# Kernel optimization log

Hardware: AMD Instinct MI355X
Metric: run time of the kernel (lower is better)

Reference implementation:

```python
import jax, jax.numpy as jnp
import numpy as np

B, L, K = 4, 1024, 48
EF, NF, NPE, NRBF, NCLS = 128, 128, 16, 16, 3
MAXREL = 32
EDGE_IN = NPE + NRBF * 25  # 416


def setup_inputs():
    key = jax.random.key(0)
    ks = jax.random.split(key, 8)
    X = jax.random.normal(ks[0], (B, L, 4, 3), jnp.float32)
    mask = jnp.ones((B, L), jnp.float32)
    R_idx = jnp.arange(B * L, dtype=jnp.int64).reshape(B, L)
    chain_labels = jax.random.randint(ks[1], (B, L), 0, 4).astype(jnp.int64)
    membrane_per_residue_labels = jax.random.randint(ks[2], (B, L), 0, NCLS).astype(jnp.int64)
    pe_w = jax.random.normal(ks[3], (2 * MAXREL + 2, NPE), jnp.float32) * 0.05
    pe_b = jax.random.normal(ks[4], (NPE,), jnp.float32) * 0.05
    edge_w = jax.random.normal(ks[5], (EDGE_IN, EF), jnp.float32) * 0.05
    ne_g = jnp.ones((EF,), jnp.float32)
    ne_b = jnp.zeros((EF,), jnp.float32)
    node_w = jax.random.normal(ks[6], (NCLS, NF), jnp.float32) * 0.05
    nn_g = jnp.ones((NF,), jnp.float32)
    nn_b = jnp.zeros((NF,), jnp.float32)
    return {"X": X, "mask": mask, "R_idx": R_idx, "chain_labels": chain_labels,
            "membrane_per_residue_labels": membrane_per_residue_labels,
            "pe_w": pe_w, "pe_b": pe_b, "edge_w": edge_w, "ne_g": ne_g, "ne_b": ne_b,
            "node_w": node_w, "nn_g": nn_g, "nn_b": nn_b}


def _rbf(D):
    mu = jnp.linspace(2.0, 22.0, NRBF)
    sigma = (22.0 - 2.0) / NRBF
    return jnp.exp(-(((D[..., None] - mu) / sigma) ** 2))


def _gather_nb(v, e_idx):
    # v: [B, L, ...] -> [B, L, K, ...] gathered along residue dim
    return jax.vmap(lambda vi, ii: vi[ii])(v, e_idx)


def _ln(x, g, b, eps=1e-5):
    mu = jnp.mean(x, -1, keepdims=True)
    var = jnp.mean((x - mu) ** 2, -1, keepdims=True)
    return (x - mu) / jnp.sqrt(var + eps) * g + b


# 24 atom-pair RBFs after the Ca-Ca (D_neighbors) one, in the original concat order
PAIRS = [("N","N"),("C","C"),("O","O"),("Cb","Cb"),("Ca","N"),("Ca","C"),("Ca","O"),
         ("Ca","Cb"),("N","C"),("N","O"),("N","Cb"),("Cb","C"),("Cb","O"),("O","C"),
         ("N","Ca"),("C","Ca"),("O","Ca"),("Cb","Ca"),("C","N"),("O","N"),("Cb","N"),
         ("C","Cb"),("O","Cb"),("C","O")]


def reference(X, mask, R_idx, chain_labels, membrane_per_residue_labels,
              pe_w, pe_b, edge_w, ne_g, ne_b, node_w, nn_g, nn_b):
    Na, Ca, Cc, Oo = X[:, :, 0], X[:, :, 1], X[:, :, 2], X[:, :, 3]
    bvec = Ca - Na
    cvec = Cc - Ca
    avec = jnp.cross(bvec, cvec)
    Cb = -0.58273431 * avec + 0.56802827 * bvec - 0.54067466 * cvec + Ca
    coords = {"N": Na, "Ca": Ca, "C": Cc, "O": Oo, "Cb": Cb}

    # masked Ca-Ca distances + kNN (single NxN pass)
    mask2 = mask[:, :, None] * mask[:, None, :]
    dX = Ca[:, :, None, :] - Ca[:, None, :, :]
    D = mask2 * jnp.sqrt(jnp.sum(dX ** 2, -1) + 1e-6)
    D_max = jnp.max(D, -1, keepdims=True)
    D_adj = D + (1.0 - mask2) * D_max
    negD, E_idx = jax.lax.top_k(-D_adj, K)
    D_neighbors = -negD  # [B, L, K]

    # gather neighbor coords once, compute the 25 RBF features on N*K pairs only
    nb = {n: _gather_nb(v, E_idx) for n, v in coords.items()}  # [B, L, K, 3]
    rbf_list = [_rbf(D_neighbors)]
    for an, bn in PAIRS:
        d = jnp.sqrt(jnp.sum((coords[an][:, :, None, :] - nb[bn]) ** 2, -1) + 1e-6)
        rbf_list.append(_rbf(d))
    RBF_all = jnp.concatenate(rbf_list, -1)  # [B, L, K, 400]

    # positional encodings on gathered offsets / chain equality
    off = R_idx[:, :, None] - _gather_nb(R_idx, E_idx)           # [B, L, K]
    E_chains = (chain_labels[:, :, None] == _gather_nb(chain_labels, E_idx)).astype(jnp.int32)
    d = jnp.clip(off + MAXREL, 0, 2 * MAXREL).astype(jnp.int32) * E_chains + (1 - E_chains) * (2 * MAXREL + 1)
    d1h = jax.nn.one_hot(d, 2 * MAXREL + 2, dtype=jnp.float32)
    E_pos = d1h @ pe_w + pe_b                                     # [B, L, K, 16]

    E = jnp.concatenate([E_pos, RBF_all], -1) @ edge_w            # [B, L, K, 128]
    E = _ln(E, ne_g, ne_b)

    C1h = jax.nn.one_hot(membrane_per_residue_labels, NCLS, dtype=jnp.float32)
    V = _ln(C1h @ node_w, nn_g, nn_b)                             # [B, L, 128]
    return V, E, E_idx
```

## Files before the change

### kernel.cpp

```cpp
#include <hip/hip_runtime.h>
#include <math.h>

#define B_ 4
#define L_ 1024
#define K_ 48
#define EF_ 128
#define NF_ 128
#define NPE_ 16
#define NRBF_ 16
#define MAXREL_ 32
#define EDGE_IN_ 416

#define V_SIZE   (B_*L_*NF_)
#define E_OFF    (V_SIZE)
#define E_SIZE   (B_*L_*K_*EF_)
#define EIDX_OFF (E_OFF + E_SIZE)

#define XH_STRIDE 232
#define SE_STRIDE 132

typedef __attribute__((ext_vector_type(8))) short bf16x8;
typedef __attribute__((ext_vector_type(4))) float f32x4;
typedef __attribute__((ext_vector_type(4))) unsigned u32x4;

__device__ const int PA_[25] = {1, 0,2,3,4, 1,1,1,1, 0,0,0, 4,4, 3, 0,2,3,4, 2,3,4, 2,3, 2};
__device__ const int PB_[25] = {1, 0,2,3,4, 0,2,3,4, 2,3,4, 2,3, 2, 1,1,1,1, 0,0,0, 4,4, 3};

__device__ __forceinline__ unsigned short f2bf(float f){
    unsigned u = __float_as_uint(f);
    unsigned r = u + 0x7fffu + ((u >> 16) & 1u);
    return (unsigned short)(r >> 16);
}

__global__ __launch_bounds__(256) void wprep_kernel(const float* __restrict__ w,
                                                    unsigned short* __restrict__ wt)
{
    int idx = blockIdx.x * 256 + threadIdx.x;
    if (idx >= EDGE_IN_ * EF_) return;
    int f = idx & 127;
    int k = idx >> 7;
    wt[f * EDGE_IN_ + k] = f2bf(w[k * EF_ + f]);
}

__global__ __launch_bounds__(128) void v_kernel(const int* __restrict__ labels,
                                                const float* __restrict__ node_w,
                                                const float* __restrict__ g,
                                                const float* __restrict__ bb,
                                                float* __restrict__ out)
{
    int gi = blockIdx.x;
    int f  = threadIdx.x;
    int lbl = labels[gi];
    float v = node_w[lbl*NF_ + f];

    __shared__ float red[2];
    __shared__ float red2[2];
    float s = v;
    #pragma unroll
    for (int m = 1; m < 64; m <<= 1) s += __shfl_xor(s, m, 64);
    if ((f & 63) == 0) red[f >> 6] = s;
    __syncthreads();
    float mu = (red[0] + red[1]) * (1.0f / NF_);
    float d = v - mu;
    float s2 = d * d;
    #pragma unroll
    for (int m = 1; m < 64; m <<= 1) s2 += __shfl_xor(s2, m, 64);
    if ((f & 63) == 0) red2[f >> 6] = s2;
    __syncthreads();
    float var = (red2[0] + red2[1]) * (1.0f / NF_);
    out[gi*NF_ + f] = d * rsqrtf(var + 1e-5f) * g[f] + bb[f];
}

__global__ __launch_bounds__(256) void topk_kernel(const float* __restrict__ X,
                                                   const float* __restrict__ mask,
                                                   float* __restrict__ out)
{
    __shared__ float sCa[L_ * 3];
    __shared__ float sM[L_];
    __shared__ unsigned hist[256];
    __shared__ float wmax[4];
    __shared__ int sSelBin;
    __shared__ unsigned sSelLo;
    __shared__ unsigned long long cand[K_];
    __shared__ unsigned sCnt;

    int gi = blockIdx.x;
    int b  = gi >> 10;
    int i  = gi & (L_ - 1);
    int tid = threadIdx.x;

    for (int idx = tid; idx < L_ * 3; idx += 256) {
        int j = idx / 3, d = idx - j * 3;
        sCa[idx] = X[(((size_t)((b << 10) + j)) * 4 + 1) * 3 + d];
    }
    for (int j = tid; j < L_; j += 256) sM[j] = mask[(b << 10) + j];
    if (tid == 0) sCnt = 0;
    __syncthreads();

    float cx = sCa[i*3+0], cy = sCa[i*3+1], cz = sCa[i*3+2];
    float mi = sM[i];

    float lmax = 0.0f;
    #pragma unroll
    for (int q = 0; q < 4; ++q) {
        int j = tid + q * 256;
        float dx = cx - sCa[j*3+0];
        float dy = cy - sCa[j*3+1];
        float dz = cz - sCa[j*3+2];
        float dist = sqrtf(dx*dx + dy*dy + dz*dz + 1e-6f);
        lmax = fmaxf(lmax, mi * sM[j] * dist);
    }
    #pragma unroll
    for (int m = 1; m < 64; m <<= 1) lmax = fmaxf(lmax, __shfl_xor(lmax, m, 64));
    if ((tid & 63) == 0) wmax[tid >> 6] = lmax;
    __syncthreads();
    float Dmax = fmaxf(fmaxf(wmax[0], wmax[1]), fmaxf(wmax[2], wmax[3]));

    unsigned long long key[4];
    bool act[4];
    #pragma unroll
    for (int q = 0; q < 4; ++q) {
        int j = tid + q * 256;
        float dx = cx - sCa[j*3+0];
        float dy = cy - sCa[j*3+1];
        float dz = cz - sCa[j*3+2];
        float dist = sqrtf(dx*dx + dy*dy + dz*dz + 1e-6f);
        float m2 = mi * sM[j];
        float Dadj = m2 * dist + (1.0f - m2) * Dmax;
        key[q] = (((unsigned long long)__float_as_uint(Dadj)) << 32) | (unsigned)j;
        act[q] = true;
    }

    unsigned r = K_ - 1;
    unsigned long long T = 0;
    const int shifts[6] = {56, 48, 40, 32, 8, 0};
    #pragma unroll 1
    for (int p = 0; p < 6; ++p) {
        int sh = shifts[p];
        hist[tid] = 0;
        __syncthreads();
        #pragma unroll
        for (int q = 0; q < 4; ++q)
            if (act[q]) atomicAdd(&hist[(unsigned)((key[q] >> sh) & 255ULL)], 1u);
        __syncthreads();
        if (tid < 64) {
            unsigned b0 = hist[tid*4+0], b1 = hist[tid*4+1], b2 = hist[tid*4+2], b3 = hist[tid*4+3];
            unsigned s0 = b0, s1 = s0 + b1, s2 = s1 + b2, s3 = s2 + b3;
            unsigned s = s3;
            #pragma unroll
            for (int m = 1; m < 64; m <<= 1) {
                unsigned o = __shfl_up(s, m, 64);
                if (tid >= m) s += o;
            }
            unsigned base = s - s3;
            hist[tid*4+0] = base + s0;
            hist[tid*4+1] = base + s1;
            hist[tid*4+2] = base + s2;
            hist[tid*4+3] = base + s3;
        }
        __syncthreads();
        unsigned lo = (tid == 0) ? 0u : hist[tid - 1];
        unsigned hi = hist[tid];
        if (r >= lo && r < hi) { sSelBin = tid; sSelLo = lo; }
        __syncthreads();
        int bsel = sSelBin;
        r -= sSelLo;
        T |= ((unsigned long long)(unsigned)bsel) << sh;
        #pragma unroll
        for (int q = 0; q < 4; ++q)
            act[q] = act[q] && ((unsigned)((key[q] >> sh) & 255ULL) == (unsigned)bsel);
        __syncthreads();
    }

    #pragma unroll
    for (int q = 0; q < 4; ++q)
        if (key[q] <= T) {
            unsigned pos = atomicAdd(&sCnt, 1u);
            cand[pos] = key[q];
        }
    __syncthreads();

    if (tid < 64) {
        unsigned long long k64 = (tid < K_) ? cand[tid] : 0xffffffffffffffffULL;
        #pragma unroll
        for (unsigned kk = 2; kk <= 64; kk <<= 1) {
            #pragma unroll
            for (unsigned jj = kk >> 1; jj > 0; jj >>= 1) {
                unsigned long long o = __shfl_xor(k64, jj, 64);
                bool lower = (tid & jj) == 0;
                bool asc   = (tid & kk) == 0;
                unsigned long long mn = (k64 < o) ? k64 : o;
                unsigned long long mx = (k64 < o) ? o : k64;
                k64 = (lower == asc) ? mn : mx;
            }
        }
        if (tid < K_)
            out[EIDX_OFF + (size_t)gi * K_ + tid] = (float)(unsigned)(k64 & 0xffffffffULL);
    }
}

__global__ __launch_bounds__(256, 5) void edge_kernel(const float* __restrict__ X,
                                                   const int* __restrict__ Ridx,
                                                   const int* __restrict__ chains,
                                                   const float* __restrict__ pe_w,
                                                   const float* __restrict__ pe_b,
                                                   const unsigned short* __restrict__ wt,
                                                   const float* __restrict__ ne_g,
                                                   const float* __restrict__ ne_b,
                                                   float* __restrict__ out)
{
    __shared__ float sAI[16];
    __shared__ float sAJ[K_][16];
    __shared__ int   sJ[K_];
    __shared__ int   sDpos[K_];
    __shared__ __align__(16) unsigned char sBuf[K_ * SE_STRIDE * 4];

    unsigned short* xh = (unsigned short*)sBuf;
    float* sE = (float*)sBuf;

    int tid = threadIdx.x;
    int gi  = blockIdx.x;
    int b   = gi >> 10;
    int i   = gi & (L_ - 1);

    if (tid < K_) sJ[tid] = (int)out[EIDX_OFF + (size_t)gi * K_ + tid];
    __syncthreads();

    if (tid < K_ + 1) {
        int r = (tid < K_) ? sJ[tid] : i;
        const float* xr = X + ((size_t)((b << 10) + r)) * 12;
        float n0=xr[0],  n1=xr[1],  n2=xr[2];
        float a0=xr[3],  a1=xr[4],  a2=xr[5];
        float c0=xr[6],  c1=xr[7],  c2=xr[8];
        float o0=xr[9],  o1=xr[10], o2=xr[11];
        float bx=a0-n0, by=a1-n1, bz=a2-n2;
        float vx=c0-a0, vy=c1-a1, vz=c2-a2;
        float ax = by*vz - bz*vy;
        float ay = bz*vx - bx*vz;
        float az = bx*vy - by*vx;
        float cb0 = -0.58273431f*ax + 0.56802827f*bx - 0.54067466f*vx + a0;
        float cb1 = -0.58273431f*ay + 0.56802827f*by - 0.54067466f*vy + a1;
        float cb2 = -0.58273431f*az + 0.56802827f*bz - 0.54067466f*vz + a2;
        float* dst = (tid < K_) ? &sAJ[tid][0] : &sAI[0];
        dst[0]=n0;  dst[1]=n1;  dst[2]=n2;
        dst[3]=a0;  dst[4]=a1;  dst[5]=a2;
        dst[6]=c0;  dst[7]=c1;  dst[8]=c2;
        dst[9]=o0;  dst[10]=o1; dst[11]=o2;
        dst[12]=cb0; dst[13]=cb1; dst[14]=cb2;
    }
    if (tid >= 64 && tid < 64 + K_) {
        int e = tid - 64;
        int j = sJ[e];
        int off  = Ridx[gi] - Ridx[(b << 10) + j];
        int same = (chains[gi] == chains[(b << 10) + j]);
        int dcl = off + MAXREL_;
        dcl = dcl < 0 ? 0 : (dcl > 2*MAXREL_ ? 2*MAXREL_ : dcl);
        sDpos[e] = same ? dcl : (2*MAXREL_ + 1);
    }
    __syncthreads();

    const int wv = tid >> 6;
    const int ln = tid & 63;
    const int lr = ln & 15;
    const int lg = ln >> 4;

    f32x4 acc[3][2];
    #pragma unroll
    for (int rf = 0; rf < 3; ++rf)
        #pragma unroll
        for (int cf = 0; cf < 2; ++cf)
            acc[rf][cf] = (f32x4){0.0f, 0.0f, 0.0f, 0.0f};

    const unsigned short* wbase0 = wt + (size_t)(wv*32 + lr) * EDGE_IN_ + lg*8;
    const unsigned short* wbase1 = wt + (size_t)(wv*32 + 16 + lr) * EDGE_IN_ + lg*8;

    #pragma unroll
    for (int h = 0; h < 2; ++h) {
        if (h == 0) {
            #pragma unroll
            for (int p = 0; p < 2; ++p) {
                int idx = tid + p * 256;
                if (idx < 384) {
                    int e = idx >> 3, cc = (idx & 7) * 2;
                    int dp = sDpos[e];
                    float v0 = pe_w[dp*NPE_ + cc]     + pe_b[cc];
                    float v1 = pe_w[dp*NPE_ + cc + 1] + pe_b[cc + 1];
                    unsigned pk;
                    asm("v_cvt_pk_bf16_f32 %0, %1, %2" : "=v"(pk) : "v"(v0), "v"(v1));
                    *(unsigned*)&xh[e * XH_STRIDE + cc] = pk;
                }
            }
            #pragma unroll
            for (int p = 0; p < 3; ++p) {
                int idx = tid + p * 256;
                if (idx < 624) {
                    int e = idx / 13, g2 = idx - e * 13;
                    float dx = sAI[PA_[g2]*3+0] - sAJ[e][PB_[g2]*3+0];
                    float dy = sAI[PA_[g2]*3+1] - sAJ[e][PB_[g2]*3+1];
                    float dz = sAI[PA_[g2]*3+2] - sAJ[e][PB_[g2]*3+2];
                    float dist = sqrtf(dx*dx + dy*dy + dz*dz + 1e-6f);
                    float t = 0.8f * dist - 1.6f;
                    unsigned pk[8];
                    #pragma unroll
                    for (int rr = 0; rr < 8; ++rr) {
                        float v0 = __expf(-t * t); t -= 1.06666672f;
                        float v1 = __expf(-t * t); t -= 1.06666672f;
                        asm("v_cvt_pk_bf16_f32 %0, %1, %2" : "=v"(pk[rr]) : "v"(v0), "v"(v1));
                    }
                    u32x4 w0 = {pk[0], pk[1], pk[2], pk[3]};
                    u32x4 w1 = {pk[4], pk[5], pk[6], pk[7]};
                    int cb = NPE_ + g2 * 16;
                    *(u32x4*)&xh[e * XH_STRIDE + cb]     = w0;
                    *(u32x4*)&xh[e * XH_STRIDE + cb + 8] = w1;
                }
            }
        } else {
            #pragma unroll
            for (int p = 0; p < 3; ++p) {
                int idx = tid + p * 256;
                if (idx < 576) {
                    int e = idx / 12, g2 = 13 + (idx - e * 12);
                    float dx = sAI[PA_[g2]*3+0] - sAJ[e][PB_[g2]*3+0];
                    float dy = sAI[PA_[g2]*3+1] - sAJ[e][PB_[g2]*3+1];
                    float dz = sAI[PA_[g2]*3+2] - sAJ[e][PB_[g2]*3+2];
                    float dist = sqrtf(dx*dx + dy*dy + dz*dz + 1e-6f);
                    float t = 0.8f * dist - 1.6f;
                    unsigned pk[8];
                    #pragma unroll
                    for (int rr = 0; rr < 8; ++rr) {
                        float v0 = __expf(-t * t); t -= 1.06666672f;
                        float v1 = __expf(-t * t); t -= 1.06666672f;
                        asm("v_cvt_pk_bf16_f32 %0, %1, %2" : "=v"(pk[rr]) : "v"(v0), "v"(v1));
                    }
                    u32x4 w0 = {pk[0], pk[1], pk[2], pk[3]};
                    u32x4 w1 = {pk[4], pk[5], pk[6], pk[7]};
                    int cb = (g2 - 13) * 16;
                    *(u32x4*)&xh[e * XH_STRIDE + cb]     = w0;
                    *(u32x4*)&xh[e * XH_STRIDE + cb + 8] = w1;
                }
            }
        }
        __syncthreads();

        const int kb  = h ? 224 : 0;
        const int nks = h ? 6 : 7;
        #pragma unroll 4
        for (int ks = 0; ks < nks; ++ks) {
            int k0 = ks * 32;
            bf16x8 a[3], bh[2];
            bh[0] = *(const bf16x8*)(wbase0 + kb + k0);
            bh[1] = *(const bf16x8*)(wbase1 + kb + k0);
            #pragma unroll
            for (int rf = 0; rf < 3; ++rf)
                a[rf] = *(const bf16x8*)&xh[(rf*16 + lr) * XH_STRIDE + k0 + lg*8];
            #pragma unroll
            for (int rf = 0; rf < 3; ++rf) {
                #pragma unroll
                for (int cf = 0; cf < 2; ++cf)
                    acc[rf][cf] = __builtin_amdgcn_mfma_f32_16x16x32_bf16(a[rf], bh[cf], acc[rf][cf], 0, 0, 0);
            }
        }
        __syncthreads();
    }

    #pragma unroll
    for (int rf = 0; rf < 3; ++rf)
        #pragma unroll
        for (int cf = 0; cf < 2; ++cf)
            #pragma unroll
            for (int r = 0; r < 4; ++r) {
                int row = rf*16 + lg*4 + r;
                int col = wv*32 + cf*16 + lr;
                sE[row * SE_STRIDE + col] = acc[rf][cf][r];
            }
    __syncthreads();

    int l16 = tid & 15;
    float gv[8], bv[8];
    #pragma unroll
    for (int q = 0; q < 8; ++q) { gv[q] = ne_g[l16*8 + q]; bv[q] = ne_b[l16*8 + q]; }

    for (int p = 0; p < 3; ++p) {
        int e = p*16 + (tid >> 4);
        float vals[8];
        #pragma unroll
        for (int q = 0; q < 8; ++q) vals[q] = sE[e * SE_STRIDE + l16*8 + q];
        float sum = 0.0f;
        #pragma unroll
        for (int q = 0; q < 8; ++q) sum += vals[q];
        #pragma unroll
        for (int m = 1; m < 16; m <<= 1) sum += __shfl_xor(sum, m, 64);
        float mu = sum * (1.0f / 128.0f);
        float s2 = 0.0f;
        #pragma unroll
        for (int q = 0; q < 8; ++q) { float d = vals[q] - mu; s2 += d * d; }
        #pragma unroll
        for (int m = 1; m < 16; m <<= 1) s2 += __shfl_xor(s2, m, 64);
        float rstd = rsqrtf(s2 * (1.0f / 128.0f) + 1e-5f);

        float* dst = out + E_OFF + (size_t)(gi * K_ + e) * EF_ + l16*8;
        f32x4 o0, o1;
        o0[0] = (vals[0] - mu) * rstd * gv[0] + bv[0];
        o0[1] = (vals[1] - mu) * rstd * gv[1] + bv[1];
        o0[2] = (vals[2] - mu) * rstd * gv[2] + bv[2];
        o0[3] = (vals[3] - mu) * rstd * gv[3] + bv[3];
        o1[0] = (vals[4] - mu) * rstd * gv[4] + bv[4];
        o1[1] = (vals[5] - mu) * rstd * gv[5] + bv[5];
        o1[2] = (vals[6] - mu) * rstd * gv[6] + bv[6];
        o1[3] = (vals[7] - mu) * rstd * gv[7] + bv[7];
        __builtin_nontemporal_store(o0, (f32x4*)dst);
        __builtin_nontemporal_store(o1, (f32x4*)(dst + 4));
    }
}

extern "C" void kernel_launch(void* const* d_in, const int* in_sizes, int n_in,
                              void* d_out, int out_size, void* d_ws, size_t ws_size,
                              hipStream_t stream)
{
    const float* X      = (const float*)d_in[0];
    const float* mask   = (const float*)d_in[1];
    const int*   Ridx   = (const int*)d_in[2];
    const int*   chains = (const int*)d_in[3];
    const int*   memb   = (const int*)d_in[4];
    const float* pe_w   = (const float*)d_in[5];
    const float* pe_b   = (const float*)d_in[6];
    const float* edge_w = (const float*)d_in[7];
    const float* ne_g   = (const float*)d_in[8];
    const float* ne_b   = (const float*)d_in[9];
    const float* node_w = (const float*)d_in[10];
    const float* nn_g   = (const float*)d_in[11];
    const float* nn_b   = (const float*)d_in[12];
    float* out = (float*)d_out;

    unsigned short* wt = (unsigned short*)d_ws;

    wprep_kernel<<<(EDGE_IN_*EF_ + 255)/256, 256, 0, stream>>>(edge_w, wt);
    v_kernel<<<B_*L_, 128, 0, stream>>>(memb, node_w, nn_g, nn_b, out);
    topk_kernel<<<B_*L_, 256, 0, stream>>>(X, mask, out);
    edge_kernel<<<B_*L_, 256, 0, stream>>>(X, Ridx, chains, pe_w, pe_b,
                                           wt, ne_g, ne_b, out);
}
```

Measured before the change: 101.9 us.

## Fuse top-k and edge kernels into one per-residue kernel with early radix exit

Merges the top-k neighbour selection kernel and the edge featurization kernel into a single kernel per residue. The selected neighbour indices go to shared memory instead of being written to global memory and read back. The shared buffer is reused for the Ca coordinates, the mask and the edge staging, which keeps LDS use within the 5-blocks-per-CU launch bound. The radix select also stops early once the selected bin holds a single key. The cost is that the top-k phase now runs under the edge kernel's occupancy and register limits.

```diff
diff --git a/kernel.cpp b/kernel.cpp
--- a/kernel.cpp
+++ b/kernel.cpp
@@ -71,23 +71,39 @@
     out[gi*NF_ + f] = d * rsqrtf(var + 1e-5f) * g[f] + bb[f];
 }
 
-__global__ __launch_bounds__(256) void topk_kernel(const float* __restrict__ X,
+__global__ __launch_bounds__(256, 5) void fused_kernel(const float* __restrict__ X,
                                                    const float* __restrict__ mask,
+                                                   const int* __restrict__ Ridx,
+                                                   const int* __restrict__ chains,
+                                                   const float* __restrict__ pe_w,
+                                                   const float* __restrict__ pe_b,
+                                                   const unsigned short* __restrict__ wt,
+                                                   const float* __restrict__ ne_g,
+                                                   const float* __restrict__ ne_b,
                                                    float* __restrict__ out)
 {
-    __shared__ float sCa[L_ * 3];
-    __shared__ float sM[L_];
+    __shared__ __align__(16) unsigned char sBuf[K_ * SE_STRIDE * 4];
+    float* sCa = (float*)sBuf;
+    float* sM  = (float*)(sBuf + 12288);
+    unsigned short* xh = (unsigned short*)sBuf;
+    float* sE = (float*)sBuf;
+
+    __shared__ float sAI[16];
+    __shared__ float sAJ[K_][16];
+    __shared__ int   sJ[K_];
+    __shared__ int   sDpos[K_];
     __shared__ unsigned hist[256];
     __shared__ float wmax[4];
     __shared__ int sSelBin;
-    __shared__ unsigned sSelLo;
+    __shared__ unsigned sSelLo, sSelCnt;
+    __shared__ unsigned long long sTkey;
     __shared__ unsigned long long cand[K_];
     __shared__ unsigned sCnt;
 
-    int gi = blockIdx.x;
-    int b  = gi >> 10;
-    int i  = gi & (L_ - 1);
     int tid = threadIdx.x;
+    int gi  = blockIdx.x;
+    int b   = gi >> 10;
+    int i   = gi & (L_ - 1);
 
     for (int idx = tid; idx < L_ * 3; idx += 256) {
         int j = idx / 3, d = idx - j * 3;
@@ -161,7 +177,7 @@
         __syncthreads();
         unsigned lo = (tid == 0) ? 0u : hist[tid - 1];
         unsigned hi = hist[tid];
-        if (r >= lo && r < hi) { sSelBin = tid; sSelLo = lo; }
+        if (r >= lo && r < hi) { sSelBin = tid; sSelLo = lo; sSelCnt = hi - lo; }
         __syncthreads();
         int bsel = sSelBin;
         r -= sSelLo;
@@ -169,6 +185,14 @@
         #pragma unroll
         for (int q = 0; q < 4; ++q)
             act[q] = act[q] && ((unsigned)((key[q] >> sh) & 255ULL) == (unsigned)bsel);
+        if (sSelCnt == 1) {
+            #pragma unroll
+            for (int q = 0; q < 4; ++q)
+                if (act[q]) sTkey = key[q];
+            __syncthreads();
+            T = sTkey;
+            break;
+        }
         __syncthreads();
     }
 
@@ -194,41 +218,17 @@
                 k64 = (lower == asc) ? mn : mx;
             }
         }
-        if (tid < K_)
-            out[EIDX_OFF + (size_t)gi * K_ + tid] = (float)(unsigned)(k64 & 0xffffffffULL);
-    }
-}
-
-__global__ __launch_bounds__(256, 5) void edge_kernel(const float* __restrict__ X,
-                                                   const int* __restrict__ Ridx,
-                                                   const int* __restrict__ chains,
-                                                   const float* __restrict__ pe_w,
-                                                   const float* __restrict__ pe_b,
-                                                   const unsigned short* __restrict__ wt,
-                                                   const float* __restrict__ ne_g,
-                                                   const float* __restrict__ ne_b,
-                                                   float* __restrict__ out)
-{
-    __shared__ float sAI[16];
-    __shared__ float sAJ[K_][16];
-    __shared__ int   sJ[K_];
-    __shared__ int   sDpos[K_];
-    __shared__ __align__(16) unsigned char sBuf[K_ * SE_STRIDE * 4];
-
-    unsigned short* xh = (unsigned short*)sBuf;
-    float* sE = (float*)sBuf;
-
-    int tid = threadIdx.x;
-    int gi  = blockIdx.x;
-    int b   = gi >> 10;
-    int i   = gi & (L_ - 1);
-
-    if (tid < K_) sJ[tid] = (int)out[EIDX_OFF + (size_t)gi * K_ + tid];
+        if (tid < K_) {
+            int j = (int)(unsigned)(k64 & 0xffffffffULL);
+            sJ[tid] = j;
+            out[EIDX_OFF + (size_t)gi * K_ + tid] = (float)j;
+        }
+    }
     __syncthreads();
 
     if (tid < K_ + 1) {
-        int r = (tid < K_) ? sJ[tid] : i;
-        const float* xr = X + ((size_t)((b << 10) + r)) * 12;
+        int rr = (tid < K_) ? sJ[tid] : i;
+        const float* xr = X + ((size_t)((b << 10) + rr)) * 12;
         float n0=xr[0],  n1=xr[1],  n2=xr[2];
         float a0=xr[3],  a1=xr[4],  a2=xr[5];
         float c0=xr[6],  c1=xr[7],  c2=xr[8];
@@ -368,10 +368,10 @@
         #pragma unroll
         for (int cf = 0; cf < 2; ++cf)
             #pragma unroll
-            for (int r = 0; r < 4; ++r) {
-                int row = rf*16 + lg*4 + r;
+            for (int r4 = 0; r4 < 4; ++r4) {
+                int row = rf*16 + lg*4 + r4;
                 int col = wv*32 + cf*16 + lr;
-                sE[row * SE_STRIDE + col] = acc[rf][cf][r];
+                sE[row * SE_STRIDE + col] = acc[rf][cf][r4];
             }
     __syncthreads();
 
@@ -436,7 +436,6 @@
 
     wprep_kernel<<<(EDGE_IN_*EF_ + 255)/256, 256, 0, stream>>>(edge_w, wt);
     v_kernel<<<B_*L_, 128, 0, stream>>>(memb, node_w, nn_g, nn_b, out);
-    topk_kernel<<<B_*L_, 256, 0, stream>>>(X, mask, out);
-    edge_kernel<<<B_*L_, 256, 0, stream>>>(X, Ridx, chains, pe_w, pe_b,
-                                           wt, ne_g, ne_b, out);
+    fused_kernel<<<B_*L_, 256, 0, stream>>>(X, mask, Ridx, chains, pe_w, pe_b,
+                                            wt, ne_g, ne_b, out);
 }
```

Result: faster. 97.85 us (-3.9%).
